# Performance work log

Measured on AMD Instinct MI355X. Metric: run time of the kernel, lower is better.

## Reference

```python
import jax, jax.numpy as jnp
import numpy as np

N, E, IN_DIM, OUT_DIM, R = 100000, 1600000, 128, 128, 8


def setup_inputs() -> dict:
    key = jax.random.key(0)
    k = jax.random.split(key, 6)
    scale_rel = np.sqrt(6.0 / (IN_DIM + OUT_DIM))  # xavier_uniform bound
    x = jax.random.normal(k[0], (N, IN_DIM), dtype=jnp.float32)
    edge_index = jax.random.randint(k[1], (2, E), 0, N, dtype=jnp.int64)
    edge_type = jax.random.randint(k[2], (E,), 0, R, dtype=jnp.int64)
    rel_weight = jax.random.uniform(k[3], (R, IN_DIM, OUT_DIM), dtype=jnp.float32,
                                    minval=-scale_rel, maxval=scale_rel)
    w_self = jax.random.uniform(k[4], (IN_DIM, OUT_DIM), dtype=jnp.float32,
                                minval=-scale_rel, maxval=scale_rel)
    b_self = jax.random.normal(k[5], (OUT_DIM,), dtype=jnp.float32) * 0.01
    return {"x": x, "edge_index": edge_index, "edge_type": edge_type,
            "rel_weight": rel_weight, "w_self": w_self, "b_self": b_self}


def reference(x, edge_index, edge_type, rel_weight, w_self, b_self):
    n = x.shape[0]
    src, dst = edge_index[0], edge_index[1]
    # self-loop term: W_self @ h_v + b
    out = x @ w_self + b_self                                  # (N, out)
    # pre-transform every node by every relation, then gather per edge.
    # equivalent to per-relation masked (x[src_r] @ W_r) + scatter_add.
    xw = jnp.einsum('ni,rio->nro', x, rel_weight)               # (N, R, out)
    msg = xw[src, edge_type]                                    # (E, out)
    agg = jax.ops.segment_sum(msg, dst, num_segments=n)         # (N, out)
    deg = jax.ops.segment_sum(jnp.ones(dst.shape[0], x.dtype), dst, num_segments=n)
    deg = jnp.clip(deg, 1.0)[:, None]                           # (N, 1)
    return jax.nn.relu(out + agg / deg)
```

## Files before the change

kernel.cpp:

```cpp
#include <hip/hip_runtime.h>
#include <hip/hip_bf16.h>

typedef __attribute__((ext_vector_type(4))) float f32x4_t;
typedef __attribute__((ext_vector_type(8))) short bf16x8_t;

#define NCLS 8

__device__ __forceinline__ float bf2f(ushort u) {
  return __uint_as_float(((unsigned)u) << 16);
}
__device__ __forceinline__ ushort f2bf(float f) {
  unsigned u = __float_as_uint(f);
  u += 0x7fffu + ((u >> 16) & 1u);
  return (ushort)(u >> 16);
}
__device__ __forceinline__ uint packbf2(float x, float y) {
  return (uint)f2bf(x) | ((uint)f2bf(y) << 16);
}

__global__ void deg2_kernel(const int* __restrict__ dst, int* __restrict__ deg2,
                            int N, long E) {
  long i = (long)blockIdx.x * blockDim.x + threadIdx.x;
  long st = (long)gridDim.x * blockDim.x;
  for (; i < E; i += st) {
    int cls = (int)((i >> 8) & (NCLS - 1));
    atomicAdd(&deg2[(size_t)cls * N + dst[i]], 1);
  }
}

__global__ void nodedeg_kernel(const int* __restrict__ deg2, int* __restrict__ nodedeg, int N) {
  int d = blockIdx.x * 256 + threadIdx.x;
  if (d >= N) return;
  int s = 0;
#pragma unroll
  for (int c = 0; c < NCLS; c++) s += deg2[(size_t)c * N + d];
  nodedeg[d] = s;
}

__global__ __launch_bounds__(256) void scan1(const int* __restrict__ deg, int* __restrict__ starts,
                                             int* __restrict__ bsum, int M) {
  __shared__ int lds[256];
  const int tid = threadIdx.x;
  const int base = blockIdx.x * 1024 + tid * 4;
  int v0 = 0, v1 = 0, v2 = 0, v3 = 0;
  if (base + 3 < M) {
    int4 q = *(const int4*)(deg + base);
    v0 = q.x; v1 = q.y; v2 = q.z; v3 = q.w;
  } else {
    if (base + 0 < M) v0 = deg[base];
    if (base + 1 < M) v1 = deg[base + 1];
    if (base + 2 < M) v2 = deg[base + 2];
    if (base + 3 < M) v3 = deg[base + 3];
  }
  int s = v0 + v1 + v2 + v3;
  lds[tid] = s;
  __syncthreads();
  for (int off = 1; off < 256; off <<= 1) {
    int t = (tid >= off) ? lds[tid - off] : 0;
    __syncthreads();
    lds[tid] += t;
    __syncthreads();
  }
  int p = lds[tid] - s;
  if (tid == 255) bsum[blockIdx.x] = lds[255];
  if (base + 0 < M) starts[base + 0] = p; p += v0;
  if (base + 1 < M) starts[base + 1] = p; p += v1;
  if (base + 2 < M) starts[base + 2] = p; p += v2;
  if (base + 3 < M) starts[base + 3] = p;
}

__global__ __launch_bounds__(256) void scan2(int* __restrict__ bsum, int nb) {
  __shared__ int lds[256];
  const int tid = threadIdx.x;
  const int base = tid * 4;
  int v[4];
#pragma unroll
  for (int j = 0; j < 4; j++) v[j] = (base + j < nb) ? bsum[base + j] : 0;
  int s = v[0] + v[1] + v[2] + v[3];
  lds[tid] = s;
  __syncthreads();
  for (int off = 1; off < 256; off <<= 1) {
    int t = (tid >= off) ? lds[tid - off] : 0;
    __syncthreads();
    lds[tid] += t;
    __syncthreads();
  }
  int p = lds[tid] - s;
#pragma unroll
  for (int j = 0; j < 4; j++) {
    if (base + j < nb) bsum[base + j] = p;
    p += v[j];
  }
}

__global__ void scan3m(int* __restrict__ starts, int* __restrict__ cursor,
                       const int* __restrict__ bsum, int M) {
  int i = blockIdx.x * 256 + threadIdx.x;
  if (i < M) {
    int v = starts[i] + bsum[i >> 10];
    starts[i] = v;
    cursor[i] = v;
  }
}

__global__ void scan3n(int* __restrict__ starts, const int* __restrict__ bsum, int M) {
  int i = blockIdx.x * 256 + threadIdx.x;
  if (i < M) starts[i] += bsum[i >> 10];
}

__global__ void fill_csr(const int* __restrict__ src, const int* __restrict__ dst,
                         const int* __restrict__ et, int* __restrict__ cursor,
                         uint* __restrict__ packed, int N, long E) {
  long i = (long)blockIdx.x * blockDim.x + threadIdx.x;
  long st = (long)gridDim.x * blockDim.x;
  for (; i < E; i += st) {
    int cls = (int)((i >> 8) & (NCLS - 1));
    int pos = atomicAdd(&cursor[(size_t)cls * N + dst[i]], 1);
    packed[pos] = ((uint)src[i] << 4) | (uint)et[i];
  }
}

__global__ void reorder_kernel(const uint* __restrict__ pin, uint* __restrict__ pout,
                               const int* __restrict__ starts2, const int* __restrict__ deg2,
                               const int* __restrict__ node_starts, int N) {
  int d = blockIdx.x * 256 + threadIdx.x;
  if (d >= N) return;
  int run = node_starts[d];
#pragma unroll
  for (int c = 0; c < NCLS; c++) {
    int s = starts2[(size_t)c * N + d];
    int len = deg2[(size_t)c * N + d];
    for (int k = 0; k < len; k++) pout[run + k] = pin[s + k];
    run += len;
  }
}

__global__ void build_wT(const float* __restrict__ rel, const float* __restrict__ wself,
                         ushort* __restrict__ wT, int R) {
  int id = blockIdx.x * blockDim.x + threadIdx.x;
  int total = (R + 1) * 128 * 128;
  if (id >= total) return;
  int r = id >> 14;
  int rem = id & 16383;
  int o = rem >> 7;
  int i = rem & 127;
  float v = (r < R) ? rel[((size_t)r << 14) + (i << 7) + o] : wself[(i << 7) + o];
  wT[id] = f2bf(v);
}

__global__ void conv_x_kernel(const float* __restrict__ x, ushort* __restrict__ xb, long n4) {
  long i = (long)blockIdx.x * blockDim.x + threadIdx.x;
  long st = (long)gridDim.x * blockDim.x;
  for (; i < n4; i += st) {
    float4 v = ((const float4*)x)[i];
    ushort4 o;
    o.x = f2bf(v.x); o.y = f2bf(v.y); o.z = f2bf(v.z); o.w = f2bf(v.w);
    ((ushort4*)xb)[i] = o;
  }
}

__global__ __launch_bounds__(256) void gather_sum(const uint* __restrict__ packed,
                                                  const int* __restrict__ node_starts,
                                                  const int* __restrict__ nodedeg,
                                                  const ushort* __restrict__ xb,
                                                  ushort* __restrict__ S,
                                                  int N) {
  const int lane = threadIdx.x & 63;
  const int d = blockIdx.x * 4 + (threadIdx.x >> 6);
  if (d >= N) return;

  const int s0 = node_starts[d];
  const int dg = nodedeg[d];
  const int e1 = s0 + dg;

  float a0x = 0, a0y = 0, a1x = 0, a1y = 0, a2x = 0, a2y = 0, a3x = 0, a3y = 0;
  float a4x = 0, a4y = 0, a5x = 0, a5y = 0, a6x = 0, a6y = 0, a7x = 0, a7y = 0;

#define ACCUM(t, vx, vy)                                  \
  switch (t) {                                            \
    case 0: a0x += vx; a0y += vy; break;                  \
    case 1: a1x += vx; a1y += vy; break;                  \
    case 2: a2x += vx; a2y += vy; break;                  \
    case 3: a3x += vx; a3y += vy; break;                  \
    case 4: a4x += vx; a4y += vy; break;                  \
    case 5: a5x += vx; a5y += vy; break;                  \
    case 6: a6x += vx; a6y += vy; break;                  \
    default: a7x += vx; a7y += vy; break;                 \
  }

  int e = s0;
  for (; e + 3 < e1; e += 4) {
    uint r0 = packed[e], r1 = packed[e + 1], r2 = packed[e + 2], r3 = packed[e + 3];
    ushort2 m0 = *(const ushort2*)(xb + (size_t)(r0 >> 4) * 128 + lane * 2);
    ushort2 m1 = *(const ushort2*)(xb + (size_t)(r1 >> 4) * 128 + lane * 2);
    ushort2 m2 = *(const ushort2*)(xb + (size_t)(r2 >> 4) * 128 + lane * 2);
    ushort2 m3 = *(const ushort2*)(xb + (size_t)(r3 >> 4) * 128 + lane * 2);
    int t0 = (int)(r0 & 15u), t1 = (int)(r1 & 15u);
    int t2 = (int)(r2 & 15u), t3 = (int)(r3 & 15u);
    ACCUM(t0, bf2f(m0.x), bf2f(m0.y));
    ACCUM(t1, bf2f(m1.x), bf2f(m1.y));
    ACCUM(t2, bf2f(m2.x), bf2f(m2.y));
    ACCUM(t3, bf2f(m3.x), bf2f(m3.y));
  }
  for (; e < e1; e++) {
    uint r0 = packed[e];
    ushort2 m0 = *(const ushort2*)(xb + (size_t)(r0 >> 4) * 128 + lane * 2);
    int t0 = (int)(r0 & 15u);
    ACCUM(t0, bf2f(m0.x), bf2f(m0.y));
  }
#undef ACCUM

  const float inv = 1.0f / (float)((dg > 1) ? dg : 1);
  uint* Sd = (uint*)(S + (size_t)d * 1024) + lane;
  __builtin_nontemporal_store(packbf2(a0x * inv, a0y * inv), Sd + 0 * 64);
  __builtin_nontemporal_store(packbf2(a1x * inv, a1y * inv), Sd + 1 * 64);
  __builtin_nontemporal_store(packbf2(a2x * inv, a2y * inv), Sd + 2 * 64);
  __builtin_nontemporal_store(packbf2(a3x * inv, a3y * inv), Sd + 3 * 64);
  __builtin_nontemporal_store(packbf2(a4x * inv, a4y * inv), Sd + 4 * 64);
  __builtin_nontemporal_store(packbf2(a5x * inv, a5y * inv), Sd + 5 * 64);
  __builtin_nontemporal_store(packbf2(a6x * inv, a6y * inv), Sd + 6 * 64);
  __builtin_nontemporal_store(packbf2(a7x * inv, a7y * inv), Sd + 7 * 64);
}

__global__ __launch_bounds__(512) void agg_gemm(const ushort* __restrict__ S,
                                                const ushort* __restrict__ xb,
                                                const ushort* __restrict__ wT,
                                                const float* __restrict__ b,
                                                float* __restrict__ out,
                                                int N, int NR) {
  __shared__ ushort smem[2][16384];

  const int tid = threadIdx.x;
  const int lane = tid & 63;
  const int wave = tid >> 6;
  const int l15 = lane & 15;
  const int l4 = lane >> 4;
  const int nodebase = blockIdx.x * 256 + wave * 32;

  int nd[2], rd[2];
  nd[0] = nodebase + l15;
  nd[1] = nodebase + 16 + l15;
  rd[0] = (nd[0] < N) ? nd[0] : (N - 1);
  rd[1] = (nd[1] < N) ? nd[1] : (N - 1);

  f32x4_t acc[2][8];
#pragma unroll
  for (int g = 0; g < 2; g++)
#pragma unroll
    for (int nt = 0; nt < 8; nt++) acc[g][nt] = {0.f, 0.f, 0.f, 0.f};

  {
    bf16x8_t sreg[4];
#pragma unroll
    for (int j = 0; j < 4; j++) {
      int c = tid + j * 512;
      sreg[j] = *(const bf16x8_t*)(wT + c * 8);
    }
#pragma unroll
    for (int j = 0; j < 4; j++) {
      int c = tid + j * 512;
      int o = c >> 4;
      int colb = (c & 15) * 16;
      int byte = o * 256 + (colb ^ ((o & 7) << 4));
      *(bf16x8_t*)((char*)smem[0] + byte) = sreg[j];
    }
  }
  __syncthreads();

  for (int r = 0; r < NR; r++) {
    bf16x8_t sf[2][4];
#pragma unroll
    for (int g = 0; g < 2; g++) {
      const ushort* srow = (r < NR - 1) ? (S + ((size_t)rd[g] * 8 + r) * 128 + l4 * 8)
                                        : (xb + (size_t)rd[g] * 128 + l4 * 8);
#pragma unroll
      for (int kk = 0; kk < 4; kk++)
        sf[g][kk] = *(const bf16x8_t*)(srow + kk * 32);
    }

    bf16x8_t sreg[4];
    const bool pf = (r + 1 < NR);
    if (pf) {
      const ushort* wsrc = wT + ((size_t)(r + 1) << 14);
#pragma unroll
      for (int j = 0; j < 4; j++) {
        int c = tid + j * 512;
        sreg[j] = *(const bf16x8_t*)(wsrc + c * 8);
      }
    }

    const char* wbuf = (const char*)smem[r & 1];
#pragma unroll
    for (int nt = 0; nt < 8; nt++) {
      bf16x8_t wf[4];
      const int row = nt * 16 + l15;
      const int swz = (row & 7) << 4;
#pragma unroll
      for (int kk = 0; kk < 4; kk++) {
        int colb = l4 * 16 + kk * 64;
        wf[kk] = *(const bf16x8_t*)(wbuf + row * 256 + (colb ^ swz));
      }
#pragma unroll
      for (int g = 0; g < 2; g++)
#pragma unroll
        for (int kk = 0; kk < 4; kk++)
          acc[g][nt] = __builtin_amdgcn_mfma_f32_16x16x32_bf16(wf[kk], sf[g][kk], acc[g][nt], 0, 0, 0);
    }

    if (pf) {
#pragma unroll
      for (int j = 0; j < 4; j++) {
        int c = tid + j * 512;
        int o = c >> 4;
        int colb = (c & 15) * 16;
        int byte = o * 256 + (colb ^ ((o & 7) << 4));
        *(bf16x8_t*)((char*)smem[(r + 1) & 1] + byte) = sreg[j];
      }
    }
    __syncthreads();
  }

#pragma unroll
  for (int g = 0; g < 2; g++) {
    if (nd[g] < N) {
#pragma unroll
      for (int nt = 0; nt < 8; nt++) {
        float4 bv = *(const float4*)(b + nt * 16 + l4 * 4);
        f32x4_t v = acc[g][nt];
        float4 o;
        o.x = fmaxf(v[0] + bv.x, 0.f);
        o.y = fmaxf(v[1] + bv.y, 0.f);
        o.z = fmaxf(v[2] + bv.z, 0.f);
        o.w = fmaxf(v[3] + bv.w, 0.f);
        *(float4*)(out + (size_t)nd[g] * 128 + nt * 16 + l4 * 4) = o;
      }
    }
  }
}

__global__ void deg_kernel(const int* __restrict__ dst, int* __restrict__ deg, long E) {
  long i = (long)blockIdx.x * blockDim.x + threadIdx.x;
  long st = (long)gridDim.x * blockDim.x;
  for (; i < E; i += st) atomicAdd(&deg[dst[i]], 1);
}
__global__ void naive_edge(const float* __restrict__ x, const int* __restrict__ src,
                           const int* __restrict__ dst, const int* __restrict__ et,
                           const float* __restrict__ rel, float* __restrict__ agg, long E) {
  const int lane = threadIdx.x & 63;
  long wid = ((long)blockIdx.x * blockDim.x + threadIdx.x) >> 6;
  long nw = ((long)gridDim.x * blockDim.x) >> 6;
  for (long e = wid; e < E; e += nw) {
    int s = src[e];
    int d = dst[e];
    int t = et[e];
    const float* xs = x + (size_t)s * 128;
    const float* w = rel + (size_t)t * 128 * 128;
    float a0 = 0.f, a1 = 0.f;
    for (int i = 0; i < 128; i++) {
      float xv = xs[i];
      a0 += xv * w[i * 128 + lane];
      a1 += xv * w[i * 128 + lane + 64];
    }
    atomicAdd(agg + (size_t)d * 128 + lane, a0);
    atomicAdd(agg + (size_t)d * 128 + lane + 64, a1);
  }
}
__global__ void naive_self(const float* __restrict__ x, const float* __restrict__ ws,
                           const float* __restrict__ b, const int* __restrict__ deg,
                           float* __restrict__ out, int N) {
  int v = blockIdx.x;
  int o = threadIdx.x;
  if (v >= N) return;
  const float* xv = x + (size_t)v * 128;
  float acc = b[o];
  for (int i = 0; i < 128; i++) acc += xv[i] * ws[i * 128 + o];
  float dg = (float)max(deg[v], 1);
  float val = acc + out[(size_t)v * 128 + o] / dg;
  out[(size_t)v * 128 + o] = fmaxf(val, 0.f);
}

extern "C" void kernel_launch(void* const* d_in, const int* in_sizes, int n_in,
                              void* d_out, int out_size, void* d_ws, size_t ws_size,
                              hipStream_t stream) {
  const float* x = (const float*)d_in[0];
  const int* ei = (const int*)d_in[1];
  const int* et = (const int*)d_in[2];
  const float* rel = (const float*)d_in[3];
  const float* wself = (const float*)d_in[4];
  const float* bself = (const float*)d_in[5];
  float* out = (float*)d_out;

  const int N = in_sizes[0] / 128;
  const long E = in_sizes[2];
  const int R = in_sizes[3] / (128 * 128);
  const int NR = R + 1;
  const int* srcp = ei;
  const int* dstp = ei + E;
  const int M = NCLS * N;

  size_t off = 0;
  auto alloc = [&](size_t bytes) {
    size_t o = off;
    off += (bytes + 255) & ~(size_t)255;
    return o;
  };
  size_t deg2_off = alloc((size_t)M * 4);
  size_t nodedeg_off = alloc((size_t)N * 4);
  size_t nstart_off = alloc((size_t)N * 4);
  size_t starts2_off = alloc((size_t)M * 4);
  size_t cursor2_off = alloc((size_t)M * 4);
  size_t bsum_off = alloc(4096);
  size_t wT_off = alloc((size_t)NR * 128 * 128 * 2);
  size_t pcls_off = alloc((size_t)E * 4);
  size_t packed_off = alloc((size_t)E * 4);
  size_t xb_off = alloc((size_t)N * 128 * 2);
  size_t S_off = alloc((size_t)N * 8 * 128 * 2);
  const bool main_path = (ws_size >= off) && (M <= 1024 * 1024) && (R == 8);

  if (main_path) {
    int* deg2 = (int*)((char*)d_ws + deg2_off);
    int* nodedeg = (int*)((char*)d_ws + nodedeg_off);
    int* nstart = (int*)((char*)d_ws + nstart_off);
    int* starts2 = (int*)((char*)d_ws + starts2_off);
    int* cursor2 = (int*)((char*)d_ws + cursor2_off);
    int* bsum = (int*)((char*)d_ws + bsum_off);
    ushort* wT = (ushort*)((char*)d_ws + wT_off);
    uint* pcls = (uint*)((char*)d_ws + pcls_off);
    uint* packed = (uint*)((char*)d_ws + packed_off);
    ushort* xb = (ushort*)((char*)d_ws + xb_off);
    ushort* S = (ushort*)((char*)d_ws + S_off);

    hipMemsetAsync(deg2, 0, (size_t)M * 4, stream);
    deg2_kernel<<<2048, 256, 0, stream>>>(dstp, deg2, N, E);
    nodedeg_kernel<<<(N + 255) / 256, 256, 0, stream>>>(deg2, nodedeg, N);

    const int nbM = (M + 1023) / 1024;
    scan1<<<nbM, 256, 0, stream>>>(deg2, starts2, bsum, M);
    scan2<<<1, 256, 0, stream>>>(bsum, nbM);
    scan3m<<<(M + 255) / 256, 256, 0, stream>>>(starts2, cursor2, bsum, M);

    const int nbN = (N + 1023) / 1024;
    scan1<<<nbN, 256, 0, stream>>>(nodedeg, nstart, bsum, N);
    scan2<<<1, 256, 0, stream>>>(bsum, nbN);
    scan3n<<<(N + 255) / 256, 256, 0, stream>>>(nstart, bsum, N);

    fill_csr<<<2048, 256, 0, stream>>>(srcp, dstp, et, cursor2, pcls, N, E);
    reorder_kernel<<<(N + 255) / 256, 256, 0, stream>>>(pcls, packed, starts2, deg2, nstart, N);

    conv_x_kernel<<<2048, 256, 0, stream>>>(x, xb, (long)N * 32);
    build_wT<<<(NR * 16384 + 255) / 256, 256, 0, stream>>>(rel, wself, wT, R);
    gather_sum<<<(N + 3) / 4, 256, 0, stream>>>(packed, nstart, nodedeg, xb, S, N);
    agg_gemm<<<(N + 255) / 256, 512, 0, stream>>>(S, xb, wT, bself, out, N, NR);
  } else {
    int* deg = (int*)((char*)d_ws + deg2_off);
    hipMemsetAsync(deg, 0, (size_t)N * 4, stream);
    deg_kernel<<<2048, 256, 0, stream>>>(dstp, deg, E);
    hipMemsetAsync(out, 0, (size_t)out_size * 4, stream);
    naive_edge<<<4096, 256, 0, stream>>>(x, srcp, dstp, et, rel, out, E);
    naive_self<<<N, 128, 0, stream>>>(x, wself, bself, deg, out, N);
  }
}
```

Before: 455.0 us.

## Merge CSR-build and prep kernels, vectorize edge reads, broadcast indices via readlane

After: 437.4 us. 1.04x faster.

```diff
diff --git a/kernel.cpp b/kernel.cpp
--- a/kernel.cpp
+++ b/kernel.cpp
@@ -20,37 +20,69 @@
 
 __global__ void deg2_kernel(const int* __restrict__ dst, int* __restrict__ deg2,
                             int N, long E) {
-  long i = (long)blockIdx.x * blockDim.x + threadIdx.x;
-  long st = (long)gridDim.x * blockDim.x;
-  for (; i < E; i += st) {
-    int cls = (int)((i >> 8) & (NCLS - 1));
-    atomicAdd(&deg2[(size_t)cls * N + dst[i]], 1);
-  }
-}
-
-__global__ void nodedeg_kernel(const int* __restrict__ deg2, int* __restrict__ nodedeg, int N) {
-  int d = blockIdx.x * 256 + threadIdx.x;
-  if (d >= N) return;
-  int s = 0;
-#pragma unroll
-  for (int c = 0; c < NCLS; c++) s += deg2[(size_t)c * N + d];
-  nodedeg[d] = s;
-}
-
-__global__ __launch_bounds__(256) void scan1(const int* __restrict__ deg, int* __restrict__ starts,
-                                             int* __restrict__ bsum, int M) {
+  const int cls = blockIdx.x & (NCLS - 1);
+  int* mydeg = deg2 + (size_t)cls * N;
+  long q = (long)blockIdx.x * blockDim.x + threadIdx.x;
+  const long nq = E >> 2;
+  const long st = (long)gridDim.x * blockDim.x;
+  for (; q < nq; q += st) {
+    int4 d4 = ((const int4*)dst)[q];
+    atomicAdd(&mydeg[d4.x], 1);
+    atomicAdd(&mydeg[d4.y], 1);
+    atomicAdd(&mydeg[d4.z], 1);
+    atomicAdd(&mydeg[d4.w], 1);
+  }
+}
+
+__global__ __launch_bounds__(256) void scan1b(const int* __restrict__ deg2,
+                                              int* __restrict__ starts2, int* __restrict__ nodedeg,
+                                              int* __restrict__ nstart, int* __restrict__ bsum,
+                                              int N, int M, int nbM) {
   __shared__ int lds[256];
   const int tid = threadIdx.x;
-  const int base = blockIdx.x * 1024 + tid * 4;
   int v0 = 0, v1 = 0, v2 = 0, v3 = 0;
-  if (base + 3 < M) {
-    int4 q = *(const int4*)(deg + base);
-    v0 = q.x; v1 = q.y; v2 = q.z; v3 = q.w;
+  int* outp;
+  int* bs;
+  int base, lim, bidx;
+  if ((int)blockIdx.x < nbM) {
+    bidx = blockIdx.x;
+    base = bidx * 1024 + tid * 4;
+    lim = M;
+    if (base + 3 < M) {
+      int4 q = *(const int4*)(deg2 + base);
+      v0 = q.x; v1 = q.y; v2 = q.z; v3 = q.w;
+    } else {
+      if (base + 0 < M) v0 = deg2[base];
+      if (base + 1 < M) v1 = deg2[base + 1];
+      if (base + 2 < M) v2 = deg2[base + 2];
+      if (base + 3 < M) v3 = deg2[base + 3];
+    }
+    outp = starts2;
+    bs = bsum;
   } else {
-    if (base + 0 < M) v0 = deg[base];
-    if (base + 1 < M) v1 = deg[base + 1];
-    if (base + 2 < M) v2 = deg[base + 2];
-    if (base + 3 < M) v3 = deg[base + 3];
+    bidx = blockIdx.x - nbM;
+    base = bidx * 1024 + tid * 4;
+    lim = N;
+    if (base + 3 < N) {
+#pragma unroll
+      for (int c = 0; c < NCLS; c++) {
+        int4 q = *(const int4*)(deg2 + (size_t)c * N + base);
+        v0 += q.x; v1 += q.y; v2 += q.z; v3 += q.w;
+      }
+      *(int4*)(nodedeg + base) = make_int4(v0, v1, v2, v3);
+    } else {
+      for (int k = 0; k < 4; k++) {
+        if (base + k < N) {
+          int s = 0;
+#pragma unroll
+          for (int c = 0; c < NCLS; c++) s += deg2[(size_t)c * N + base + k];
+          if (k == 0) v0 = s; else if (k == 1) v1 = s; else if (k == 2) v2 = s; else v3 = s;
+          nodedeg[base + k] = s;
+        }
+      }
+    }
+    outp = nstart;
+    bs = bsum + 1024;
   }
   int s = v0 + v1 + v2 + v3;
   lds[tid] = s;
@@ -62,20 +94,22 @@
     __syncthreads();
   }
   int p = lds[tid] - s;
-  if (tid == 255) bsum[blockIdx.x] = lds[255];
-  if (base + 0 < M) starts[base + 0] = p; p += v0;
-  if (base + 1 < M) starts[base + 1] = p; p += v1;
-  if (base + 2 < M) starts[base + 2] = p; p += v2;
-  if (base + 3 < M) starts[base + 3] = p;
-}
-
-__global__ __launch_bounds__(256) void scan2(int* __restrict__ bsum, int nb) {
+  if (tid == 255) bs[bidx] = lds[255];
+  if (base + 0 < lim) outp[base + 0] = p; p += v0;
+  if (base + 1 < lim) outp[base + 1] = p; p += v1;
+  if (base + 2 < lim) outp[base + 2] = p; p += v2;
+  if (base + 3 < lim) outp[base + 3] = p;
+}
+
+__global__ __launch_bounds__(256) void scan2b(int* __restrict__ bsum, int nbM, int nbN) {
   __shared__ int lds[256];
+  int* b = bsum + blockIdx.x * 1024;
+  const int nb = (blockIdx.x == 0) ? nbM : nbN;
   const int tid = threadIdx.x;
   const int base = tid * 4;
   int v[4];
 #pragma unroll
-  for (int j = 0; j < 4; j++) v[j] = (base + j < nb) ? bsum[base + j] : 0;
+  for (int j = 0; j < 4; j++) v[j] = (base + j < nb) ? b[base + j] : 0;
   int s = v[0] + v[1] + v[2] + v[3];
   lds[tid] = s;
   __syncthreads();
@@ -88,35 +122,45 @@
   int p = lds[tid] - s;
 #pragma unroll
   for (int j = 0; j < 4; j++) {
-    if (base + j < nb) bsum[base + j] = p;
+    if (base + j < nb) b[base + j] = p;
     p += v[j];
   }
 }
 
-__global__ void scan3m(int* __restrict__ starts, int* __restrict__ cursor,
-                       const int* __restrict__ bsum, int M) {
+__global__ void scan3b(int* __restrict__ starts2, int* __restrict__ cursor2,
+                       int* __restrict__ nstart, const int* __restrict__ bsum,
+                       int M, int N) {
   int i = blockIdx.x * 256 + threadIdx.x;
   if (i < M) {
-    int v = starts[i] + bsum[i >> 10];
-    starts[i] = v;
-    cursor[i] = v;
-  }
-}
-
-__global__ void scan3n(int* __restrict__ starts, const int* __restrict__ bsum, int M) {
-  int i = blockIdx.x * 256 + threadIdx.x;
-  if (i < M) starts[i] += bsum[i >> 10];
+    int v = starts2[i] + bsum[i >> 10];
+    starts2[i] = v;
+    cursor2[i] = v;
+  } else if (i < M + N) {
+    int j = i - M;
+    nstart[j] += bsum[1024 + (j >> 10)];
+  }
 }
 
 __global__ void fill_csr(const int* __restrict__ src, const int* __restrict__ dst,
                          const int* __restrict__ et, int* __restrict__ cursor,
                          uint* __restrict__ packed, int N, long E) {
-  long i = (long)blockIdx.x * blockDim.x + threadIdx.x;
-  long st = (long)gridDim.x * blockDim.x;
-  for (; i < E; i += st) {
-    int cls = (int)((i >> 8) & (NCLS - 1));
-    int pos = atomicAdd(&cursor[(size_t)cls * N + dst[i]], 1);
-    packed[pos] = ((uint)src[i] << 4) | (uint)et[i];
+  const int cls = blockIdx.x & (NCLS - 1);
+  int* mycur = cursor + (size_t)cls * N;
+  long q = (long)blockIdx.x * blockDim.x + threadIdx.x;
+  const long nq = E >> 2;
+  const long st = (long)gridDim.x * blockDim.x;
+  for (; q < nq; q += st) {
+    int4 s4 = ((const int4*)src)[q];
+    int4 d4 = ((const int4*)dst)[q];
+    int4 t4 = ((const int4*)et)[q];
+    int p0 = atomicAdd(&mycur[d4.x], 1);
+    packed[p0] = ((uint)s4.x << 4) | (uint)t4.x;
+    int p1 = atomicAdd(&mycur[d4.y], 1);
+    packed[p1] = ((uint)s4.y << 4) | (uint)t4.y;
+    int p2 = atomicAdd(&mycur[d4.z], 1);
+    packed[p2] = ((uint)s4.z << 4) | (uint)t4.z;
+    int p3 = atomicAdd(&mycur[d4.w], 1);
+    packed[p3] = ((uint)s4.w << 4) | (uint)t4.w;
   }
 }
 
@@ -135,27 +179,29 @@
   }
 }
 
-__global__ void build_wT(const float* __restrict__ rel, const float* __restrict__ wself,
-                         ushort* __restrict__ wT, int R) {
-  int id = blockIdx.x * blockDim.x + threadIdx.x;
-  int total = (R + 1) * 128 * 128;
-  if (id >= total) return;
-  int r = id >> 14;
-  int rem = id & 16383;
-  int o = rem >> 7;
-  int i = rem & 127;
-  float v = (r < R) ? rel[((size_t)r << 14) + (i << 7) + o] : wself[(i << 7) + o];
-  wT[id] = f2bf(v);
-}
-
-__global__ void conv_x_kernel(const float* __restrict__ x, ushort* __restrict__ xb, long n4) {
+__global__ void prep_kernel(const float* __restrict__ rel, const float* __restrict__ wself,
+                            ushort* __restrict__ wT, const float* __restrict__ x,
+                            ushort* __restrict__ xb, int R, long n4) {
+  const long total_wT = (long)(R + 1) * 16384;
+  const long total = total_wT + n4;
   long i = (long)blockIdx.x * blockDim.x + threadIdx.x;
-  long st = (long)gridDim.x * blockDim.x;
-  for (; i < n4; i += st) {
-    float4 v = ((const float4*)x)[i];
-    ushort4 o;
-    o.x = f2bf(v.x); o.y = f2bf(v.y); o.z = f2bf(v.z); o.w = f2bf(v.w);
-    ((ushort4*)xb)[i] = o;
+  const long st = (long)gridDim.x * blockDim.x;
+  for (; i < total; i += st) {
+    if (i < total_wT) {
+      int id = (int)i;
+      int r = id >> 14;
+      int rem = id & 16383;
+      int o = rem >> 7;
+      int ii = rem & 127;
+      float v = (r < R) ? rel[((size_t)r << 14) + (ii << 7) + o] : wself[(ii << 7) + o];
+      wT[id] = f2bf(v);
+    } else {
+      long j = i - total_wT;
+      float4 v = ((const float4*)x)[j];
+      ushort4 o;
+      o.x = f2bf(v.x); o.y = f2bf(v.y); o.z = f2bf(v.z); o.w = f2bf(v.w);
+      ((ushort4*)xb)[j] = o;
+    }
   }
 }
 
@@ -172,42 +218,69 @@
   const int s0 = node_starts[d];
   const int dg = nodedeg[d];
   const int e1 = s0 + dg;
+  const int voff = lane * 2;
 
   float a0x = 0, a0y = 0, a1x = 0, a1y = 0, a2x = 0, a2y = 0, a3x = 0, a3y = 0;
   float a4x = 0, a4y = 0, a5x = 0, a5y = 0, a6x = 0, a6y = 0, a7x = 0, a7y = 0;
 
-#define ACCUM(t, vx, vy)                                  \
-  switch (t) {                                            \
-    case 0: a0x += vx; a0y += vy; break;                  \
-    case 1: a1x += vx; a1y += vy; break;                  \
-    case 2: a2x += vx; a2y += vy; break;                  \
-    case 3: a3x += vx; a3y += vy; break;                  \
-    case 4: a4x += vx; a4y += vy; break;                  \
-    case 5: a5x += vx; a5y += vy; break;                  \
-    case 6: a6x += vx; a6y += vy; break;                  \
-    default: a7x += vx; a7y += vy; break;                 \
+#define ROWLOAD(r) (*(const ushort2*)(xb + (size_t)((r) >> 4) * 128 + voff))
+#define ACCUM(t, m)                                                       \
+  {                                                                       \
+    float vx = bf2f((m).x), vy = bf2f((m).y);                             \
+    switch (t) {                                                          \
+      case 0: a0x += vx; a0y += vy; break;                                \
+      case 1: a1x += vx; a1y += vy; break;                                \
+      case 2: a2x += vx; a2y += vy; break;                                \
+      case 3: a3x += vx; a3y += vy; break;                                \
+      case 4: a4x += vx; a4y += vy; break;                                \
+      case 5: a5x += vx; a5y += vy; break;                                \
+      case 6: a6x += vx; a6y += vy; break;                                \
+      default: a7x += vx; a7y += vy; break;                               \
+    }                                                                     \
   }
 
   int e = s0;
-  for (; e + 3 < e1; e += 4) {
-    uint r0 = packed[e], r1 = packed[e + 1], r2 = packed[e + 2], r3 = packed[e + 3];
-    ushort2 m0 = *(const ushort2*)(xb + (size_t)(r0 >> 4) * 128 + lane * 2);
-    ushort2 m1 = *(const ushort2*)(xb + (size_t)(r1 >> 4) * 128 + lane * 2);
-    ushort2 m2 = *(const ushort2*)(xb + (size_t)(r2 >> 4) * 128 + lane * 2);
-    ushort2 m3 = *(const ushort2*)(xb + (size_t)(r3 >> 4) * 128 + lane * 2);
-    int t0 = (int)(r0 & 15u), t1 = (int)(r1 & 15u);
-    int t2 = (int)(r2 & 15u), t3 = (int)(r3 & 15u);
-    ACCUM(t0, bf2f(m0.x), bf2f(m0.y));
-    ACCUM(t1, bf2f(m1.x), bf2f(m1.y));
-    ACCUM(t2, bf2f(m2.x), bf2f(m2.y));
-    ACCUM(t3, bf2f(m3.x), bf2f(m3.y));
-  }
-  for (; e < e1; e++) {
-    uint r0 = packed[e];
-    ushort2 m0 = *(const ushort2*)(xb + (size_t)(r0 >> 4) * 128 + lane * 2);
-    int t0 = (int)(r0 & 15u);
-    ACCUM(t0, bf2f(m0.x), bf2f(m0.y));
-  }
+#pragma unroll 1
+  for (; e + 7 < e1; e += 8) {
+    uint v = packed[e + (lane & 7)];
+    uint r0 = (uint)__builtin_amdgcn_readlane((int)v, 0);
+    uint r1 = (uint)__builtin_amdgcn_readlane((int)v, 1);
+    uint r2 = (uint)__builtin_amdgcn_readlane((int)v, 2);
+    uint r3 = (uint)__builtin_amdgcn_readlane((int)v, 3);
+    uint r4 = (uint)__builtin_amdgcn_readlane((int)v, 4);
+    uint r5 = (uint)__builtin_amdgcn_readlane((int)v, 5);
+    uint r6 = (uint)__builtin_amdgcn_readlane((int)v, 6);
+    uint r7 = (uint)__builtin_amdgcn_readlane((int)v, 7);
+    ushort2 m0 = ROWLOAD(r0);
+    ushort2 m1 = ROWLOAD(r1);
+    ushort2 m2 = ROWLOAD(r2);
+    ushort2 m3 = ROWLOAD(r3);
+    ushort2 m4 = ROWLOAD(r4);
+    ushort2 m5 = ROWLOAD(r5);
+    ushort2 m6 = ROWLOAD(r6);
+    ushort2 m7 = ROWLOAD(r7);
+    ACCUM((int)(r0 & 15u), m0);
+    ACCUM((int)(r1 & 15u), m1);
+    ACCUM((int)(r2 & 15u), m2);
+    ACCUM((int)(r3 & 15u), m3);
+    ACCUM((int)(r4 & 15u), m4);
+    ACCUM((int)(r5 & 15u), m5);
+    ACCUM((int)(r6 & 15u), m6);
+    ACCUM((int)(r7 & 15u), m7);
+  }
+  const int rem = e1 - e;
+  if (rem > 0) {
+    uint v = packed[e + (lane & 7)];
+    uint r0 = (uint)__builtin_amdgcn_readlane((int)v, 0);
+    { ushort2 m = ROWLOAD(r0); ACCUM((int)(r0 & 15u), m); }
+    if (rem > 1) { uint r = (uint)__builtin_amdgcn_readlane((int)v, 1); ushort2 m = ROWLOAD(r); ACCUM((int)(r & 15u), m); }
+    if (rem > 2) { uint r = (uint)__builtin_amdgcn_readlane((int)v, 2); ushort2 m = ROWLOAD(r); ACCUM((int)(r & 15u), m); }
+    if (rem > 3) { uint r = (uint)__builtin_amdgcn_readlane((int)v, 3); ushort2 m = ROWLOAD(r); ACCUM((int)(r & 15u), m); }
+    if (rem > 4) { uint r = (uint)__builtin_amdgcn_readlane((int)v, 4); ushort2 m = ROWLOAD(r); ACCUM((int)(r & 15u), m); }
+    if (rem > 5) { uint r = (uint)__builtin_amdgcn_readlane((int)v, 5); ushort2 m = ROWLOAD(r); ACCUM((int)(r & 15u), m); }
+    if (rem > 6) { uint r = (uint)__builtin_amdgcn_readlane((int)v, 6); ushort2 m = ROWLOAD(r); ACCUM((int)(r & 15u), m); }
+  }
+#undef ROWLOAD
 #undef ACCUM
 
   const float inv = 1.0f / (float)((dg > 1) ? dg : 1);
@@ -409,13 +482,14 @@
   size_t nstart_off = alloc((size_t)N * 4);
   size_t starts2_off = alloc((size_t)M * 4);
   size_t cursor2_off = alloc((size_t)M * 4);
-  size_t bsum_off = alloc(4096);
+  size_t bsum_off = alloc(8192);
   size_t wT_off = alloc((size_t)NR * 128 * 128 * 2);
   size_t pcls_off = alloc((size_t)E * 4);
   size_t packed_off = alloc((size_t)E * 4);
   size_t xb_off = alloc((size_t)N * 128 * 2);
   size_t S_off = alloc((size_t)N * 8 * 128 * 2);
-  const bool main_path = (ws_size >= off) && (M <= 1024 * 1024) && (R == 8);
+  const bool main_path = (ws_size >= off) && (M <= 1024 * 1024) && (R == 8) &&
+                         ((E & 3) == 0) && ((N & 3) == 0);
 
   if (main_path) {
     int* deg2 = (int*)((char*)d_ws + deg2_off);
@@ -432,23 +506,16 @@
 
     hipMemsetAsync(deg2, 0, (size_t)M * 4, stream);
     deg2_kernel<<<2048, 256, 0, stream>>>(dstp, deg2, N, E);
-    nodedeg_kernel<<<(N + 255) / 256, 256, 0, stream>>>(deg2, nodedeg, N);
 
     const int nbM = (M + 1023) / 1024;
-    scan1<<<nbM, 256, 0, stream>>>(deg2, starts2, bsum, M);
-    scan2<<<1, 256, 0, stream>>>(bsum, nbM);
-    scan3m<<<(M + 255) / 256, 256, 0, stream>>>(starts2, cursor2, bsum, M);
-
     const int nbN = (N + 1023) / 1024;
-    scan1<<<nbN, 256, 0, stream>>>(nodedeg, nstart, bsum, N);
-    scan2<<<1, 256, 0, stream>>>(bsum, nbN);
-    scan3n<<<(N + 255) / 256, 256, 0, stream>>>(nstart, bsum, N);
+    scan1b<<<nbM + nbN, 256, 0, stream>>>(deg2, starts2, nodedeg, nstart, bsum, N, M, nbM);
+    scan2b<<<2, 256, 0, stream>>>(bsum, nbM, nbN);
+    scan3b<<<(M + N + 255) / 256, 256, 0, stream>>>(starts2, cursor2, nstart, bsum, M, N);
 
     fill_csr<<<2048, 256, 0, stream>>>(srcp, dstp, et, cursor2, pcls, N, E);
     reorder_kernel<<<(N + 255) / 256, 256, 0, stream>>>(pcls, packed, starts2, deg2, nstart, N);
-
-    conv_x_kernel<<<2048, 256, 0, stream>>>(x, xb, (long)N * 32);
-    build_wT<<<(NR * 16384 + 255) / 256, 256, 0, stream>>>(rel, wself, wT, R);
+    prep_kernel<<<2048, 256, 0, stream>>>(rel, wself, wT, x, xb, R, (long)N * 32);
     gather_sum<<<(N + 3) / 4, 256, 0, stream>>>(packed, nstart, nodedeg, xb, S, N);
     agg_gemm<<<(N + 255) / 256, 512, 0, stream>>>(S, xb, wT, bself, out, N, NR);
   } else {
```
